# Kernel optimization log

Measured on AMD Instinct MI355X. Metric: run time of the kernel, lower is better.

The kernel has to match this reference:

```python
import jax, jax.numpy as jnp
import numpy as np

B, C, H, W = 256, 512, 14, 14
HW = H * W
TAU = 0.03          # args.tau
EPS = 0.65          # args.epsilon
EPS2 = 0.40         # args.epsilon - args.epsilon_margin
T_LOGIT = 0.07      # args.logit_temperature
MAX_ITERS = 32      # static unrolled bound for the data-dependent while-loop
PD_EPS = 1e-6       # torch.nn.PairwiseDistance default eps (added to the difference)


def setup_inputs() -> dict:
    key = jax.random.key(0)
    k1, k2 = jax.random.split(key)
    img = jax.random.normal(k1, (B, C, H, W), jnp.float32)
    img = img / (jnp.linalg.norm(img, axis=1, keepdims=True) + 1e-12)  # L2 over channels
    aud = jax.random.normal(k2, (B, C), jnp.float32)
    aud = aud / (jnp.linalg.norm(aud, axis=1, keepdims=True) + 1e-12)
    return {"img": img, "aud": aud}


def reference(img, aud):
    Bb, Cc, Hh, Ww = img.shape
    n_pix = Hh * Ww

    # PosLogits: [B,1,H,W]; Alllogits: [B,B,H,W]
    pos_logits = jnp.einsum('ncqa,nc->nqa', img, aud)[:, None]
    all_logits = jnp.einsum('ncqa,kc->nkqa', img, aud)

    # trimap negatives
    pos2 = jax.nn.sigmoid((pos_logits - EPS2) / TAU)
    neg = 1.0 - pos2                                        # [B,1,H,W]

    logit = img.reshape(Bb, Cc, -1) * pos_logits.reshape(Bb, 1, -1)   # [B,C,HW]
    positive0 = pos_logits.reshape(Bb, -1)                            # [B,HW]
    neg_val = (logit * neg.reshape(Bb, 1, -1)).mean(axis=2)           # [B,C]

    logit_t = logit.transpose(0, 2, 1)                                 # [B,HW,C]
    dist_to_zero = jnp.linalg.norm(logit_t - neg_val[:, None, :] + PD_EPS, axis=-1)  # [B,HW]

    def body(t, state):
        positive, already_pos, endpoint, obj = state
        idx = jnp.argmax(positive, axis=1)                             # [B] (detached in torch)
        sel = jnp.take_along_axis(logit, idx[:, None, None], axis=2)[:, :, 0]  # [B,C]
        obj = obj.at[t].set(sel * (~endpoint)[:, None].astype(sel.dtype))
        dist_to_logit = jnp.linalg.norm(logit_t - sel[:, None, :] + PD_EPS, axis=-1)  # [B,HW]
        pos = (dist_to_logit < dist_to_zero) & (~already_pos)
        already_pos = already_pos | pos
        positive = positive * (1.0 - pos.astype(positive.dtype))
        endpoint = endpoint | (pos.sum(axis=1) == 0) | (positive.max(axis=1) < 0.1)
        return (positive, already_pos, endpoint, obj)

    obj0 = jnp.zeros((MAX_ITERS, Bb, Cc), img.dtype)
    state0 = (positive0,
              jnp.zeros((Bb, n_pix), bool),
              jnp.zeros((Bb,), bool),
              obj0)
    _, _, _, object_arr = jax.lax.fori_loop(0, MAX_ITERS, body, state0)

    # lvs contrastive loss
    mask = 1.0 - 100.0 * jnp.eye(Bb, dtype=img.dtype)
    pos_m = jax.nn.sigmoid((pos_logits - EPS) / TAU)                   # [B,1,H,W]
    pos_all = jax.nn.sigmoid((all_logits - EPS) / TAU)                 # [B,B,H,W]
    sim1 = (pos_m * pos_logits).reshape(Bb, 1, -1).sum(-1) / pos_m.reshape(Bb, 1, -1).sum(-1)
    sim = (pos_all * all_logits).reshape(Bb, Bb, -1).sum(-1) / pos_all.reshape(Bb, Bb, -1).sum(-1) * mask
    sim2 = (neg * pos_logits).reshape(Bb, 1, -1).sum(-1) / neg.reshape(Bb, 1, -1).sum(-1)
    logits = jnp.concatenate((sim1, sim, sim2), axis=1) / T_LOGIT      # [B, B+2]
    loss = -jax.nn.log_softmax(logits, axis=1)[:, 0].mean()           # CE with target 0

    return loss, pos_logits[:, 0], object_arr
```

## Files before the change

### kernel.cpp

```cpp
#include <hip/hip_runtime.h>
#include <hip/hip_bf16.h>
#include <math.h>

#define NB 256
#define NC 512
#define NP 196
#define NIT 32
#define PROWS 208

typedef __attribute__((ext_vector_type(8))) short bf16x8;
typedef __attribute__((ext_vector_type(4))) float f32x4;

__device__ __forceinline__ float sigf(float z){ return 1.0f/(1.0f+expf(-z)); }

__device__ __forceinline__ unsigned short f2bf(float x){
  return __bfloat16_as_ushort(__float2bfloat16(x));
}
__device__ __forceinline__ float bf2f(unsigned short h){
  union{float f; unsigned u;} v; v.u = ((unsigned)h)<<16; return v.f;
}
__device__ __forceinline__ double dshfl_xor(double v, int m){
  int lo = __shfl_xor(__double2loint(v), m);
  int hi = __shfl_xor(__double2hiint(v), m);
  return __hiloint2double(hi, lo);
}

__global__ __launch_bounds__(256) void aud2bf_kernel(const float* __restrict__ aud, unsigned short* __restrict__ aud_bf)
{
  int i = blockIdx.x*256 + threadIdx.x;
  aud_bf[i] = f2bf(aud[i]);
}


#define SFSTR 211
__global__ __launch_bounds__(512) void convert3_kernel(
    const float* __restrict__ img, const float* __restrict__ aud,
    unsigned short* __restrict__ hiT, unsigned short* __restrict__ loT,
    double* __restrict__ ppl, double* __restrict__ pcs)
{
  const int bid = blockIdx.x;
  const int b = bid & 255, part = bid >> 8;
  const int tid = threadIdx.x;
  const float* imgb = img + (size_t)b*NC*NP;
  __shared__ float sf[32*SFSTR];
  __shared__ double s_dp[PROWS], s_ds[PROWS];
  __shared__ float s_aud[128];
  if (tid < 128) s_aud[tid] = aud[b*NC + part*128 + tid];
  for (int i=tid;i<PROWS;i+=512){ s_dp[i]=0.0; s_ds[i]=0.0; }

  for (int ss=0; ss<4; ++ss){
    const int c0 = part*128 + ss*32;
    __syncthreads();
    for (int j=tid; j<32*49; j+=512){
      int p4 = j % 49, c = j / 49;
      float4 v = *(const float4*)&imgb[(size_t)(c0+c)*NP + p4*4];
      sf[c*SFSTR + p4*4+0]=v.x; sf[c*SFSTR + p4*4+1]=v.y;
      sf[c*SFSTR + p4*4+2]=v.z; sf[c*SFSTR + p4*4+3]=v.w;
    }
    __syncthreads();
    for (int j=tid; j<PROWS*4; j+=512){
      int p = j >> 2, cq = j & 3;
      unsigned hv[4], lv[4];
      double dot=0.0, sm=0.0;
      #pragma unroll
      for (int k2=0;k2<4;++k2){
        float x0 = (p<NP) ? sf[(cq*8+2*k2  )*SFSTR + p] : 0.f;
        float x1 = (p<NP) ? sf[(cq*8+2*k2+1)*SFSTR + p] : 0.f;
        unsigned short h0=f2bf(x0), h1=f2bf(x1);
        unsigned short l0=f2bf(x0-bf2f(h0)), l1=f2bf(x1-bf2f(h1));
        hv[k2] = (unsigned)h0 | ((unsigned)h1<<16);
        lv[k2] = (unsigned)l0 | ((unsigned)l1<<16);
        int ca = ss*32 + cq*8 + 2*k2;
        dot += (double)x0*(double)s_aud[ca] + (double)x1*(double)s_aud[ca+1];
        sm  += (double)x0 + (double)x1;
      }
      size_t o = ((size_t)b*PROWS + p)*NC + c0 + cq*8;
      *(uint4*)&hiT[o] = *(uint4*)hv;
      *(uint4*)&loT[o] = *(uint4*)lv;
      dot += dshfl_xor(dot,1); dot += dshfl_xor(dot,2);
      sm  += dshfl_xor(sm,1);  sm  += dshfl_xor(sm,2);
      if (cq==0 && p<NP){ s_dp[p] += dot; s_ds[p] += sm; }
    }
  }
  __syncthreads();
  for (int i=tid;i<NP;i+=512){
    ppl[((size_t)b*4 + part)*NP + i] = s_dp[i];
    pcs[((size_t)b*4 + part)*NP + i] = s_ds[i];
  }
}

__global__ __launch_bounds__(256) void prep3_kernel(
    const double* __restrict__ ppl, const double* __restrict__ pcs,
    float* __restrict__ pl, float* __restrict__ cs,
    float* __restrict__ sim1, float* __restrict__ sim2, float* __restrict__ out_pl)
{
  const int b = blockIdx.x, tid = threadIdx.x;
  __shared__ double s_redd[256];
  float plv=0.f;
  if (tid < NP){
    double a=0.0, s=0.0;
    #pragma unroll
    for (int part=0; part<4; ++part){
      a += ppl[((size_t)b*4+part)*NP + tid];
      s += pcs[((size_t)b*4+part)*NP + tid];
    }
    plv=(float)a;
    float csv=(float)s;
    pl[b*NP+tid]=plv; cs[b*NP+tid]=csv; out_pl[b*NP+tid]=plv;
  }
  float pmw = (tid<NP)? sigf((plv-0.65f)/0.03f) : 0.f;
  float negw= (tid<NP)? 1.0f - sigf((plv-0.40f)/0.03f) : 0.f;
  double r[4];
  r[0]=(tid<NP)?(double)pmw*(double)plv:0.0;
  r[1]=(tid<NP)?(double)pmw:0.0;
  r[2]=(tid<NP)?(double)negw*(double)plv:0.0;
  r[3]=(tid<NP)?(double)negw:0.0;
  double res[4];
  for (int i=0;i<4;++i){
    __syncthreads();
    s_redd[tid]=r[i];
    __syncthreads();
    for (int s=128;s>0;s>>=1){ if (tid<s) s_redd[tid]+=s_redd[tid+s]; __syncthreads(); }
    res[i]=s_redd[0];
  }
  if (tid==0){
    sim1[b]=(float)(res[0]/res[1]);
    sim2[b]=(float)(res[2]/res[3]);
  }
}

#define LSTR 72
__global__ __launch_bounds__(512) void gram2_kernel(
    const unsigned short* __restrict__ hiT, const unsigned short* __restrict__ loT,
    float* __restrict__ G)
{
  const int bid = blockIdx.x;
  const int b = bid & 255, h = bid >> 8;
  const int cbase = 7*h, ncl = 7 - h;
  const int tid = threadIdx.x, lane = tid & 63, w = tid >> 6;
  const int nr = (w<5)?2:1;
  const unsigned short* hb = hiT + (size_t)b*PROWS*NC;
  const unsigned short* lb = loT + (size_t)b*PROWS*NC;
  float* Gb = G + (size_t)b*NP*NP;
  __shared__ short smh[PROWS*LSTR];
  __shared__ short sml[PROWS*LSTR];

  f32x4 acc[2][7];
  #pragma unroll
  for (int i=0;i<2;++i)
    #pragma unroll
    for (int j=0;j<7;++j) acc[i][j]=(f32x4){0,0,0,0};

  for (int sl=0; sl<8; ++sl){
    __syncthreads();
    for (int j=tid; j<PROWS*8; j+=512){
      int p = j>>3, o = j&7;
      size_t src = (size_t)p*NC + sl*64 + o*8;
      uint4 hv = *(const uint4*)(hb + src);
      uint4 lv = *(const uint4*)(lb + src);
      *(uint4*)&smh[p*LSTR + o*8] = hv;
      *(uint4*)&sml[p*LSTR + o*8] = lv;
    }
    __syncthreads();
    #pragma unroll
    for (int kk=0; kk<2; ++kk){
      bf16x8 Ah[2], Al[2];
      #pragma unroll
      for (int i=0;i<2;++i){
        if (i<nr){
          int r = (w + 8*i)*16 + (lane&15);
          Ah[i] = *(const bf16x8*)&smh[r*LSTR + kk*32 + (lane>>4)*8];
          Al[i] = *(const bf16x8*)&sml[r*LSTR + kk*32 + (lane>>4)*8];
        }
      }
      #pragma unroll
      for (int j=0;j<7;++j){
        if (j<ncl){
          int r = (cbase+j)*16 + (lane&15);
          bf16x8 Bh = *(const bf16x8*)&smh[r*LSTR + kk*32 + (lane>>4)*8];
          bf16x8 Bl = *(const bf16x8*)&sml[r*LSTR + kk*32 + (lane>>4)*8];
          #pragma unroll
          for (int i=0;i<2;++i){
            if (i<nr){
              acc[i][j] = __builtin_amdgcn_mfma_f32_16x16x32_bf16(Ah[i], Bh, acc[i][j], 0,0,0);
              acc[i][j] = __builtin_amdgcn_mfma_f32_16x16x32_bf16(Ah[i], Bl, acc[i][j], 0,0,0);
              acc[i][j] = __builtin_amdgcn_mfma_f32_16x16x32_bf16(Al[i], Bh, acc[i][j], 0,0,0);
            }
          }
        }
      }
    }
  }

  const int r0 = (lane>>4)*4, colL = lane & 15;
  #pragma unroll
  for (int i=0;i<2;++i){
    #pragma unroll
    for (int j=0;j<7;++j){
      if (i<nr && j<ncl){
        int row = (w+8*i)*16 + r0;
        int col = (cbase+j)*16 + colL;
        if (col < NP){
          #pragma unroll
          for (int jj=0;jj<4;++jj){
            if (row+jj < NP) Gb[(size_t)(row+jj)*NP + col] = acc[i][j][jj];
          }
        }
      }
    }
  }
}

__global__ __launch_bounds__(512) void simgemm2_kernel(
    const unsigned short* __restrict__ hiT, const unsigned short* __restrict__ aud_bf,
    float* __restrict__ sumWA, float* __restrict__ sumW)
{
  const int bid = blockIdx.x;
  const int b = bid & 255, h = bid >> 8;
  const int tid = threadIdx.x, lane = tid & 63, w = tid >> 6;
  const int wr = w >> 2, wc = w & 3;
  const int pbase = (wr==0)?0:7, npt = 7-wr;
  const unsigned short* hb = hiT + (size_t)b*PROWS*NC;
  __shared__ short smh[PROWS*LSTR];
  __shared__ short sma[128*LSTR];
  __shared__ float sred[2][2][4][2][16];

  f32x4 acc[7][2];
  #pragma unroll
  for (int i=0;i<7;++i)
    #pragma unroll
    for (int n=0;n<2;++n) acc[i][n]=(f32x4){0,0,0,0};

  for (int sl=0; sl<8; ++sl){
    __syncthreads();
    for (int j=tid; j<PROWS*8; j+=512){
      int p = j>>3, o = j&7;
      *(uint4*)&smh[p*LSTR + o*8] = *(const uint4*)(hb + (size_t)p*NC + sl*64 + o*8);
    }
    for (int j=tid; j<128*8; j+=512){
      int n = j>>3, o = j&7;
      *(uint4*)&sma[n*LSTR + o*8] = *(const uint4*)(aud_bf + (size_t)(h*128+n)*NC + sl*64 + o*8);
    }
    __syncthreads();
    #pragma unroll
    for (int kk=0; kk<2; ++kk){
      bf16x8 Ah[7];
      #pragma unroll
      for (int i=0;i<7;++i){
        if (i<npt){
          int r = (pbase+i)*16 + (lane&15);
          Ah[i] = *(const bf16x8*)&smh[r*LSTR + kk*32 + (lane>>4)*8];
        }
      }
      #pragma unroll
      for (int n=0;n<2;++n){
        int r = (wc*2+n)*16 + (lane&15);
        bf16x8 Bn = *(const bf16x8*)&sma[r*LSTR + kk*32 + (lane>>4)*8];
        #pragma unroll
        for (int i=0;i<7;++i)
          if (i<npt)
            acc[i][n] = __builtin_amdgcn_mfma_f32_16x16x32_bf16(Ah[i], Bn, acc[i][n], 0,0,0);
      }
    }
  }

  float swa[2]={0,0}, sw[2]={0,0};
  #pragma unroll
  for (int n=0;n<2;++n){
    #pragma unroll
    for (int i=0;i<7;++i){
      if (i<npt){
        int rowbase = (pbase+i)*16 + (lane>>4)*4;
        #pragma unroll
        for (int jj=0;jj<4;++jj){
          if (rowbase+jj < NP){
            float v = acc[i][n][jj];
            float wgt = sigf((v-0.65f)/0.03f);
            swa[n] += wgt*v; sw[n] += wgt;
          }
        }
      }
    }
  }
  #pragma unroll
  for (int n=0;n<2;++n){
    swa[n] += __shfl_xor(swa[n],16); swa[n] += __shfl_xor(swa[n],32);
    sw[n]  += __shfl_xor(sw[n],16);  sw[n]  += __shfl_xor(sw[n],32);
  }
  if (lane < 16){
    #pragma unroll
    for (int n=0;n<2;++n){
      sred[0][wr][wc][n][lane] = swa[n];
      sred[1][wr][wc][n][lane] = sw[n];
    }
  }
  __syncthreads();
  if (tid < 128){
    int wc2 = tid>>5, n2 = (tid>>4)&1, col = tid&15;
    float a = sred[0][0][wc2][n2][col] + sred[0][1][wc2][n2][col];
    float s = sred[1][0][wc2][n2][col] + sred[1][1][wc2][n2][col];
    int kcol = h*128 + (wc2*2+n2)*16 + col;
    sumWA[(size_t)b*NB + kcol] = a;
    sumW [(size_t)b*NB + kcol] = s;
  }
}

__global__ __launch_bounds__(256) void loop3_kernel(
    const float* __restrict__ pl, const float* __restrict__ cs,
    const float* __restrict__ G, int* __restrict__ qseq, int* __restrict__ zf)
{
  const int b = blockIdx.x, tid = threadIdx.x, lane = tid & 63, w = tid >> 6;
  const float* Gb = G + (size_t)b*NP*NP;
  __shared__ float sG[NP*NP];
  __shared__ float s_pl[NP], s_wl[NP], s_csL[NP], s_gd[NP];
  __shared__ double gwd[NP];
  __shared__ double s_redd[256];

  #pragma unroll
  for (int k=0;k<38;++k){
    int j = k*256 + tid;
    if (j < NP*NP/4) ((float4*)sG)[j] = ((const float4*)Gb)[j];
  }
  float negw_t = 0.f;
  if (tid < NP){
    float plv = pl[b*NP+tid];
    float csv = cs[b*NP+tid];
    s_pl[tid] = plv;
    s_csL[tid] = plv*csv;
    negw_t = 1.0f - sigf((plv-0.40f)/0.03f);
    s_wl[tid] = plv*negw_t;
    s_gd[tid] = Gb[(size_t)tid*NP + tid];
  }
  __syncthreads();

  double gw = 0.0;
  if (tid < NP){
    for (int q=0;q<NP;++q) gw += (double)sG[q*NP + tid] * (double)s_wl[q];
    gwd[tid] = gw;
  }
  __syncthreads();
  s_redd[tid] = (tid<NP) ? (double)s_wl[tid]*gw : 0.0;
  __syncthreads();
  for (int st=128;st>0;st>>=1){ if (tid<st) s_redd[tid]+=s_redd[tid+st]; __syncthreads(); }
  const double S2 = s_redd[0];
  __syncthreads();
  s_redd[tid] = (tid<NP) ? (double)negw_t*(double)s_csL[tid] : 0.0;
  __syncthreads();
  for (int st=128;st>0;st>>=1){ if (tid<st) s_redd[tid]+=s_redd[tid+st]; __syncthreads(); }
  const double Swl = s_redd[0];
  __syncthreads();

  if (tid < NP){
    const double e = (double)1e-6f;
    double pld = (double)s_pl[tid];
    double d0sq = pld*pld*(double)s_gd[tid]
                - (2.0/196.0)*pld*gwd[tid]
                + S2/(196.0*196.0)
                + 2.0*e*((double)s_csL[tid] - Swl/196.0)
                + 512.0*e*e;
    if (d0sq < 0.0) d0sq = 0.0;
    gwd[tid] = d0sq;
  }
  __syncthreads();

  if (w != 0) return;

  float plv[4], csL[4], gdd[4], posv[4];
  double d0sq[4];
  bool alr[4];
  #pragma unroll
  for (int s=0;s<4;++s){
    int p = lane + 64*s;
    bool valid = p < NP;
    plv[s]  = valid ? s_pl[p]  : 0.f;
    csL[s]  = valid ? s_csL[p] : 0.f;
    gdd[s]  = valid ? s_gd[p]  : 0.f;
    d0sq[s] = valid ? gwd[p]   : 0.0;
    posv[s] = valid ? plv[s]   : -INFINITY;
    alr[s] = false;
  }
  bool endp = false;

  for (int t=0;t<NIT;++t){
    float v = posv[0]; int ix = lane;
    #pragma unroll
    for (int s=1;s<4;++s){
      if (posv[s] > v){ v = posv[s]; ix = lane + 64*s; }
    }
    #pragma unroll
    for (int m=1;m<64;m<<=1){
      float vv = __shfl_xor(v, m);
      int   ii = __shfl_xor(ix, m);
      if (vv>v || (vv==v && ii<ix)){ v=vv; ix=ii; }
    }
    const int q = ix;
    const float plq  = s_pl[q];
    const float gqq  = s_gd[q];
    const float csLq = s_csL[q];
    if (lane==0){ qseq[b*NIT+t] = q; zf[b*NIT+t] = endp ? 1 : 0; }

    int cnt = 0;
    #pragma unroll
    for (int s=0;s<4;++s){
      int p = lane + 64*s;
      if (p<NP && !alr[s]){
        float Gpq = sG[q*NP + p];
        double plp=(double)plv[s], dq=(double)plq;
        const double e=(double)1e-6f;
        double d2 = plp*plp*(double)gdd[s]
                  - 2.0*plp*dq*(double)Gpq
                  + dq*dq*(double)gqq
                  + 2.0*e*((double)csL[s]-(double)csLq)
                  + 512.0*e*e;
        if (d2<0.0) d2=0.0;
        if (d2 < d0sq[s]){ alr[s]=true; posv[s]=posv[s]*0.0f; cnt++; }
      }
    }
    float mx = fmaxf(fmaxf(posv[0],posv[1]),fmaxf(posv[2],posv[3]));
    #pragma unroll
    for (int m=1;m<64;m<<=1){
      cnt += __shfl_xor(cnt, m);
      mx = fmaxf(mx, __shfl_xor(mx, m));
    }
    if (cnt==0 || mx<0.1f) endp=true;
  }
}

__global__ __launch_bounds__(64) void objw_kernel(
    const unsigned short* __restrict__ hiT, const unsigned short* __restrict__ loT,
    const float* __restrict__ pl, const int* __restrict__ qseq, const int* __restrict__ zf,
    float* __restrict__ obj)
{
  const int bid = blockIdx.x;
  const int b = bid >> 5, t = bid & 31;
  const int lane = threadIdx.x;
  float* op = obj + ((size_t)t*NB + b)*NC;
  const int z = zf[b*NIT + t];
  if (z){
    float4 zv = {0.f,0.f,0.f,0.f};
    *(float4*)&op[lane*8]   = zv;
    *(float4*)&op[lane*8+4] = zv;
    return;
  }
  const int q = qseq[b*NIT + t];
  const float plq = pl[b*NP + q];
  size_t src = ((size_t)b*PROWS + q)*NC + lane*8;
  uint4 hv = *(const uint4*)(hiT + src);
  uint4 lv = *(const uint4*)(loT + src);
  const unsigned* hw = (const unsigned*)&hv;
  const unsigned* lw = (const unsigned*)&lv;
  float o8[8];
  #pragma unroll
  for (int k2=0;k2<4;++k2){
    float x0 = bf2f((unsigned short)(hw[k2]&0xffff)) + bf2f((unsigned short)(lw[k2]&0xffff));
    float x1 = bf2f((unsigned short)(hw[k2]>>16))    + bf2f((unsigned short)(lw[k2]>>16));
    o8[2*k2]   = x0*plq;
    o8[2*k2+1] = x1*plq;
  }
  *(float4*)&op[lane*8]   = *(float4*)&o8[0];
  *(float4*)&op[lane*8+4] = *(float4*)&o8[4];
}

__global__ __launch_bounds__(256) void finalize_b(
    const float* __restrict__ sim1, const float* __restrict__ sim2,
    const float* __restrict__ sumWA, const float* __restrict__ sumW,
    float* __restrict__ lossb)
{
  const int b = blockIdx.x, k = threadIdx.x;
  __shared__ float s_red[256];
  __shared__ double s_redd[256];
  const float T = 0.07f;
  float s = sumWA[(size_t)b*NB+k]/sumW[(size_t)b*NB+k];
  if (k==b) s *= -99.0f;
  const float lk = s/T;
  const float l0 = sim1[b]/T, ll = sim2[b]/T;
  s_red[k]=lk; __syncthreads();
  for (int st=128;st>0;st>>=1){ if(k<st) s_red[k]=fmaxf(s_red[k],s_red[k+st]); __syncthreads(); }
  const float m = fmaxf(s_red[0], fmaxf(l0,ll));
  __syncthreads();
  double e = (double)expf(lk-m);
  if (k==0) e += (double)expf(l0-m)+(double)expf(ll-m);
  s_redd[k]=e; __syncthreads();
  for (int st=128;st>0;st>>=1){ if(k<st) s_redd[k]+=s_redd[k+st]; __syncthreads(); }
  if (k==0) lossb[b] = -(float)((double)(l0-m) - log(s_redd[0]));
}

__global__ __launch_bounds__(256) void finalize_sum(const float* __restrict__ lossb, float* __restrict__ out_loss)
{
  const int tid = threadIdx.x;
  __shared__ double sr[256];
  sr[tid]=(double)lossb[tid]; __syncthreads();
  for (int st=128;st>0;st>>=1){ if(tid<st) sr[tid]+=sr[tid+st]; __syncthreads(); }
  if (tid==0) out_loss[0]=(float)(sr[0]/256.0);
}


__global__ __launch_bounds__(256) void prep_fb(
    const float* __restrict__ img, const float* __restrict__ aud,
    float* __restrict__ pl, float* __restrict__ cs, float* __restrict__ d0,
    float* __restrict__ sim1, float* __restrict__ sim2,
    float* __restrict__ out_pl)
{
  const int b = blockIdx.x, tid = threadIdx.x;
  const float* imgb = img + (size_t)b*NC*NP;
  __shared__ float s_aud[NC];
  __shared__ float s_wl[NP];
  __shared__ float s_nv[NC];
  __shared__ double s_redd[256];
  for (int c=tid;c<NC;c+=256) s_aud[c]=aud[b*NC+c];
  __syncthreads();
  float plv=0.f, pmw=0.f, negw=0.f;
  if (tid<NP){
    double a=0.0, s=0.0;
    for (int c=0;c<NC;++c){ float x=imgb[(size_t)c*NP+tid]; a += (double)x*(double)s_aud[c]; s += (double)x; }
    plv=(float)a;
    float csv=(float)s;
    pl[b*NP+tid]=plv; cs[b*NP+tid]=csv; out_pl[b*NP+tid]=plv;
    pmw  = sigf((plv-0.65f)/0.03f);
    negw = 1.0f - sigf((plv-0.40f)/0.03f);
    s_wl[tid]=plv*negw;
  }
  double r[4];
  r[0]=(tid<NP)?(double)pmw*(double)plv:0.0;
  r[1]=(tid<NP)?(double)pmw:0.0;
  r[2]=(tid<NP)?(double)negw*(double)plv:0.0;
  r[3]=(tid<NP)?(double)negw:0.0;
  double res[4];
  for (int i=0;i<4;++i){
    __syncthreads();
    s_redd[tid]=r[i];
    __syncthreads();
    for (int s=128;s>0;s>>=1){ if (tid<s) s_redd[tid]+=s_redd[tid+s]; __syncthreads(); }
    res[i]=s_redd[0];
  }
  if (tid==0){
    sim1[b]=(float)(res[0]/res[1]);
    sim2[b]=(float)(res[2]/res[3]);
  }
  __syncthreads();
  for (int c=tid;c<NC;c+=256){
    const float* row = imgb + (size_t)c*NP;
    double a=0.0;
    for (int p=0;p<NP;++p) a += (double)row[p]*(double)s_wl[p];
    s_nv[c]=(float)(a/(double)NP);
  }
  __syncthreads();
  if (tid<NP){
    double a=0.0;
    const double e=(double)1e-6f;
    for (int c=0;c<NC;++c){
      double t=(double)imgb[(size_t)c*NP+tid]*(double)plv - (double)s_nv[c] + e;
      a += t*t;
    }
    d0[b*NP+tid]=(float)sqrt(a);
  }
}

#define GKS 64
#define GSTR 72
#define SKS 128
#define SSTR 136

__device__ __forceinline__ bf16x8 frag_ld(const short* sm, int stride, int tile, int kk, int lane){
  int r = tile*16 + (lane & 15);
  int o = lane >> 4;
  const short* p = sm + r*stride + kk*32 + o*8;
  return *(const bf16x8*)p;
}

__global__ __launch_bounds__(512) void gram_fb(const float* __restrict__ img, float* __restrict__ G)
{
  const int b = blockIdx.x;
  const int tid = threadIdx.x, lane = tid & 63, w = tid >> 6;
  const int wr = w >> 1, wc = w & 1;
  const int rbase = (wr==0)?0:(3*wr+1), nr = (wr==0)?4:3;
  const int cbase = 7*wc, ncl = 7-wc;
  const float* imgb = img + (size_t)b*NC*NP;
  float* Gb = G + (size_t)b*NP*NP;
  __shared__ short smh[PROWS*GSTR];
  __shared__ short sml[PROWS*GSTR];

  f32x4 acc[4][7];
  #pragma unroll
  for (int i=0;i<4;++i)
    #pragma unroll
    for (int j=0;j<7;++j) acc[i][j] = (f32x4){0.f,0.f,0.f,0.f};

  for (int sl=0; sl<NC/GKS; ++sl){
    __syncthreads();
    #pragma unroll
    for (int it=0; it<4; ++it){
      int j = it*512 + tid;
      int p = j & 255, c8 = j >> 8;
      if (p < PROWS){
        float x[8];
        #pragma unroll
        for (int cc=0;cc<8;++cc){
          int c = sl*GKS + c8*8 + cc;
          x[cc] = (p<NP) ? imgb[(size_t)c*NP + p] : 0.f;
        }
        unsigned hw[4], lw[4];
        #pragma unroll
        for (int k2=0;k2<4;++k2){
          unsigned short h0=f2bf(x[2*k2]), h1=f2bf(x[2*k2+1]);
          float l0 = x[2*k2]-bf2f(h0), l1 = x[2*k2+1]-bf2f(h1);
          hw[k2] = (unsigned)h0 | ((unsigned)h1<<16);
          lw[k2] = (unsigned)f2bf(l0) | ((unsigned)f2bf(l1)<<16);
        }
        *(uint4*)&smh[p*GSTR + c8*8] = *(uint4*)hw;
        *(uint4*)&sml[p*GSTR + c8*8] = *(uint4*)lw;
      }
    }
    __syncthreads();
    #pragma unroll
    for (int kk=0; kk<GKS/32; ++kk){
      bf16x8 Ah[4], Al[4];
      #pragma unroll
      for (int i=0;i<4;++i){
        if (i<nr){ Ah[i]=frag_ld(smh,GSTR,rbase+i,kk,lane); Al[i]=frag_ld(sml,GSTR,rbase+i,kk,lane); }
      }
      #pragma unroll
      for (int j=0;j<7;++j){
        if (j<ncl){
          bf16x8 Bh = frag_ld(smh,GSTR,cbase+j,kk,lane);
          bf16x8 Bl = frag_ld(sml,GSTR,cbase+j,kk,lane);
          #pragma unroll
          for (int i=0;i<4;++i){
            if (i<nr){
              acc[i][j] = __builtin_amdgcn_mfma_f32_16x16x32_bf16(Ah[i], Bh, acc[i][j], 0,0,0);
              acc[i][j] = __builtin_amdgcn_mfma_f32_16x16x32_bf16(Ah[i], Bl, acc[i][j], 0,0,0);
              acc[i][j] = __builtin_amdgcn_mfma_f32_16x16x32_bf16(Al[i], Bh, acc[i][j], 0,0,0);
            }
          }
        }
      }
    }
  }

  const int r0 = (lane>>4)*4, colL = lane & 15;
  #pragma unroll
  for (int i=0;i<4;++i){
    #pragma unroll
    for (int j=0;j<7;++j){
      if (i<nr && j<ncl){
        int row = (rbase+i)*16 + r0;
        int col = (cbase+j)*16 + colL;
        if (col < NP){
          #pragma unroll
          for (int jj=0;jj<4;++jj){
            if (row+jj < NP) Gb[(size_t)(row+jj)*NP + col] = acc[i][j][jj];
          }
        }
      }
    }
  }
}

__global__ __launch_bounds__(512) void simgemm_fb(
    const float* __restrict__ img, const unsigned short* __restrict__ aud_bf,
    float* __restrict__ sumWA, float* __restrict__ sumW)
{
  const int b = blockIdx.x;
  const int tid = threadIdx.x, lane = tid & 63, w = tid >> 6;
  const int wr = w >> 2, wc = w & 3;
  const int pbase = (wr==0)?0:7, npt = 7-wr;
  const float* imgb = img + (size_t)b*NC*NP;
  __shared__ short smh[PROWS*SSTR];
  __shared__ float sred[2][2][4][4][16];

  f32x4 acc[7][4];
  #pragma unroll
  for (int i=0;i<7;++i)
    #pragma unroll
    for (int n=0;n<4;++n) acc[i][n] = (f32x4){0.f,0.f,0.f,0.f};

  for (int sl=0; sl<NC/SKS; ++sl){
    __syncthreads();
    #pragma unroll
    for (int it=0; it<8; ++it){
      int j = it*512 + tid;
      int p = j & 255, c8 = j >> 8;
      if (p < PROWS){
        float x[8];
        #pragma unroll
        for (int cc=0;cc<8;++cc){
          int c = sl*SKS + c8*8 + cc;
          x[cc] = (p<NP) ? imgb[(size_t)c*NP + p] : 0.f;
        }
        unsigned hw[4];
        #pragma unroll
        for (int k2=0;k2<4;++k2)
          hw[k2] = (unsigned)f2bf(x[2*k2]) | ((unsigned)f2bf(x[2*k2+1])<<16);
        *(uint4*)&smh[p*SSTR + c8*8] = *(uint4*)hw;
      }
    }
    __syncthreads();
    #pragma unroll
    for (int kk=0; kk<SKS/32; ++kk){
      bf16x8 Ah[7];
      #pragma unroll
      for (int i=0;i<7;++i)
        if (i<npt) Ah[i]=frag_ld(smh,SSTR,pbase+i,kk,lane);
      #pragma unroll
      for (int n=0;n<4;++n){
        int ntile = wc*4 + n;
        int k = ntile*16 + (lane&15);
        int c = sl*SKS + kk*32 + (lane>>4)*8;
        bf16x8 Bn = *(const bf16x8*)(aud_bf + (size_t)k*NC + c);
        #pragma unroll
        for (int i=0;i<7;++i)
          if (i<npt)
            acc[i][n] = __builtin_amdgcn_mfma_f32_16x16x32_bf16(Ah[i], Bn, acc[i][n], 0,0,0);
      }
    }
  }

  float swa[4]={0,0,0,0}, sw[4]={0,0,0,0};
  #pragma unroll
  for (int n=0;n<4;++n){
    #pragma unroll
    for (int i=0;i<7;++i){
      if (i<npt){
        int rowbase = (pbase+i)*16 + (lane>>4)*4;
        #pragma unroll
        for (int jj=0;jj<4;++jj){
          if (rowbase+jj < NP){
            float v = acc[i][n][jj];
            float wgt = sigf((v-0.65f)/0.03f);
            swa[n] += wgt*v; sw[n] += wgt;
          }
        }
      }
    }
  }
  #pragma unroll
  for (int n=0;n<4;++n){
    swa[n] += __shfl_xor(swa[n],16); swa[n] += __shfl_xor(swa[n],32);
    sw[n]  += __shfl_xor(sw[n],16);  sw[n]  += __shfl_xor(sw[n],32);
  }
  if (lane < 16){
    #pragma unroll
    for (int n=0;n<4;++n){
      sred[0][wr][wc][n][lane] = swa[n];
      sred[1][wr][wc][n][lane] = sw[n];
    }
  }
  __syncthreads();
  if (tid < 256){
    int wc2 = tid>>6, n2 = (tid>>4)&3, col = tid&15;
    float a = sred[0][0][wc2][n2][col] + sred[0][1][wc2][n2][col];
    float s = sred[1][0][wc2][n2][col] + sred[1][1][wc2][n2][col];
    sumWA[(size_t)b*NB + tid] = a;
    sumW [(size_t)b*NB + tid] = s;
  }
}

__global__ __launch_bounds__(64) void loop_fb(
    const float* __restrict__ img, const float* __restrict__ pl,
    const float* __restrict__ cs, const float* __restrict__ d0,
    const float* __restrict__ G, float* __restrict__ obj)
{
  const int b = blockIdx.x, lane = threadIdx.x;
  const float* imgb = img + (size_t)b*NC*NP;
  const float* Gb = G + (size_t)b*NP*NP;

  float plv[4], csL[4], d0v[4], gdd[4], posv[4];
  bool alr[4];
  #pragma unroll
  for (int s=0;s<4;++s){
    int p = lane + 64*s;
    bool valid = p < NP;
    plv[s] = valid ? pl[b*NP+p] : 0.f;
    csL[s] = valid ? plv[s]*cs[b*NP+p] : 0.f;
    d0v[s] = valid ? d0[b*NP+p] : 0.f;
    gdd[s] = valid ? Gb[(size_t)p*NP+p] : 0.f;
    posv[s] = valid ? plv[s] : -INFINITY;
    alr[s] = false;
  }
  bool endp = false;

  for (int t=0;t<NIT;++t){
    float v = posv[0]; int ix = lane;
    #pragma unroll
    for (int s=1;s<4;++s){
      if (posv[s] > v){ v = posv[s]; ix = lane + 64*s; }
    }
    #pragma unroll
    for (int m=1;m<64;m<<=1){
      float vv = __shfl_xor(v, m);
      int   ii = __shfl_xor(ix, m);
      if (vv>v || (vv==v && ii<ix)){ v=vv; ix=ii; }
    }
    const int q = ix;
    const int slot = q >> 6, ln = q & 63;
    float pq=0.f, gq=0.f, cq=0.f;
    #pragma unroll
    for (int s=0;s<4;++s){
      if (s==slot){ pq=plv[s]; gq=gdd[s]; cq=csL[s]; }
    }
    const float plq  = __shfl(pq, ln);
    const float gqq  = __shfl(gq, ln);
    const float csLq = __shfl(cq, ln);

    {
      float* op = obj + ((size_t)t*NB + b)*NC;
      #pragma unroll
      for (int j2=0;j2<8;++j2){
        int c = lane + 64*j2;
        op[c] = endp ? 0.0f : imgb[(size_t)c*NP + q]*plq;
      }
    }

    int cnt = 0;
    #pragma unroll
    for (int s=0;s<4;++s){
      int p = lane + 64*s;
      if (p<NP && !alr[s]){
        float Gpq = Gb[(size_t)q*NP + p];
        double plp=(double)plv[s], dq=(double)plq;
        const double e=(double)1e-6f;
        double d2 = plp*plp*(double)gdd[s]
                  - 2.0*plp*dq*(double)Gpq
                  + dq*dq*(double)gqq
                  + 2.0*e*((double)csL[s]-(double)csLq)
                  + (double)NC*e*e;
        if (d2<0.0) d2=0.0;
        if (sqrt(d2) < (double)d0v[s]){ alr[s]=true; posv[s]=posv[s]*0.0f; cnt++; }
      }
    }
    float mx = fmaxf(fmaxf(posv[0],posv[1]),fmaxf(posv[2],posv[3]));
    #pragma unroll
    for (int m=1;m<64;m<<=1){
      cnt += __shfl_xor(cnt, m);
      mx = fmaxf(mx, __shfl_xor(mx, m));
    }
    if (cnt==0 || mx<0.1f) endp=true;
  }
}

__global__ __launch_bounds__(256) void finalize_fb(
    const float* __restrict__ sim1, const float* __restrict__ sim2,
    const float* __restrict__ sumWA, const float* __restrict__ sumW,
    float* __restrict__ out_loss)
{
  const int b = threadIdx.x;
  const float T = 0.07f;
  float l0 = sim1[b]/T;
  float ll = sim2[b]/T;
  float m = fmaxf(l0,ll);
  for (int k=0;k<NB;++k){
    float s = sumWA[(size_t)b*NB+k]/sumW[(size_t)b*NB+k];
    if (k==b) s *= -99.0f;
    m = fmaxf(m, s/T);
  }
  double se = exp((double)(l0-m)) + exp((double)(ll-m));
  for (int k=0;k<NB;++k){
    float s = sumWA[(size_t)b*NB+k]/sumW[(size_t)b*NB+k];
    if (k==b) s *= -99.0f;
    se += exp((double)(s/T-m));
  }
  float lsm0 = (float)((double)(l0-m) - log(se));
  __shared__ double s_redd[256];
  s_redd[b] = -(double)lsm0;
  __syncthreads();
  for (int s=128;s>0;s>>=1){ if (b<s) s_redd[b]+=s_redd[b+s]; __syncthreads(); }
  if (b==0) out_loss[0]=(float)(s_redd[0]/(double)NB);
}

extern "C" void kernel_launch(void* const* d_in, const int* in_sizes, int n_in,
                              void* d_out, int out_size, void* d_ws, size_t ws_size,
                              hipStream_t stream)
{
  const float* img = (const float*)d_in[0];
  const float* aud = (const float*)d_in[1];
  float* out = (float*)d_out;
  float* ws  = (float*)d_ws;

  float* pl    = ws;
  float* cs    = pl    + NB*NP;
  float* d0    = cs    + NB*NP;
  float* sim1  = d0    + NB*NP;
  float* sim2  = sim1  + NB;
  float* sumWA = sim2  + NB;
  float* sumW  = sumWA + NB*NB;
  unsigned short* aud_bf = (unsigned short*)(sumW + NB*NB);
  float* G     = (float*)(aud_bf + NB*NC);
  unsigned short* hiT = (unsigned short*)(G + (size_t)NB*NP*NP);
  unsigned short* loT = hiT + (size_t)NB*PROWS*NC;
  int* qseq    = (int*)(loT + (size_t)NB*PROWS*NC);
  int* zf      = qseq + NB*NIT;
  float* lossb = (float*)(zf + NB*NIT);

  double* ppl = (double*)G;
  double* pcs = ppl + (size_t)NB*4*NP;

  const size_t need_fast = (size_t)((char*)(lossb + NB) - (char*)ws);

  float* out_loss = out;
  float* out_pl   = out + 1;
  float* out_obj  = out + 1 + NB*NP;

  hipLaunchKernelGGL(aud2bf_kernel, dim3(NB*NC/256), dim3(256), 0, stream, aud, aud_bf);

  if (ws_size >= need_fast){
    hipLaunchKernelGGL(convert3_kernel, dim3(NB*4),   dim3(512), 0, stream, img, aud, hiT, loT, ppl, pcs);
    hipLaunchKernelGGL(prep3_kernel,    dim3(NB),     dim3(256), 0, stream, ppl, pcs, pl, cs, sim1, sim2, out_pl);
    hipLaunchKernelGGL(gram2_kernel,    dim3(NB*2),   dim3(512), 0, stream, hiT, loT, G);
    hipLaunchKernelGGL(loop3_kernel,    dim3(NB),     dim3(256), 0, stream, pl, cs, G, qseq, zf);
    hipLaunchKernelGGL(simgemm2_kernel, dim3(NB*2),   dim3(512), 0, stream, hiT, aud_bf, sumWA, sumW);
    hipLaunchKernelGGL(objw_kernel,     dim3(NB*NIT), dim3(64),  0, stream, hiT, loT, pl, qseq, zf, out_obj);
    hipLaunchKernelGGL(finalize_b,      dim3(NB),     dim3(256), 0, stream, sim1, sim2, sumWA, sumW, lossb);
    hipLaunchKernelGGL(finalize_sum,    dim3(1),      dim3(256), 0, stream, lossb, out_loss);
  } else {
    hipLaunchKernelGGL(prep_fb,    dim3(NB), dim3(256), 0, stream, img, aud, pl, cs, d0, sim1, sim2, out_pl);
    hipLaunchKernelGGL(gram_fb,    dim3(NB), dim3(512), 0, stream, img, G);
    hipLaunchKernelGGL(simgemm_fb, dim3(NB), dim3(512), 0, stream, img, aud_bf, sumWA, sumW);
    hipLaunchKernelGGL(loop_fb,    dim3(NB), dim3(64),  0, stream, img, pl, cs, d0, G, out_obj);
    hipLaunchKernelGGL(finalize_fb,dim3(1),  dim3(256), 0, stream, sim1, sim2, sumWA, sumW, out_loss);
  }
}
```

Measured before the change: 211.6 us.

## Interleave bf16 hi/lo split planes into one packed 32-bit panel

The separate hi and lo bf16 transposed arrays are merged into a single array holding the hi and lo halves of each element in one 32-bit word. The convert kernel writes this packed panel, and the gram, simgemm and object-gather kernels load it and unpack the hi/lo fragments in registers with shift and mask operations. The aim is one contiguous global stream and one shared-memory tile, using an odd stride to avoid bank conflicts. In exchange, simgemm now loads twice the bytes it needs, since it only uses the hi part, and every fragment read pays extra unpacking ALU work.

```diff
diff --git a/kernel.cpp b/kernel.cpp
--- a/kernel.cpp
+++ b/kernel.cpp
@@ -7,6 +7,7 @@
 #define NP 196
 #define NIT 32
 #define PROWS 208
+#define USTR 65
 
 typedef __attribute__((ext_vector_type(8))) short bf16x8;
 typedef __attribute__((ext_vector_type(4))) float f32x4;
@@ -25,6 +26,27 @@
   return __hiloint2double(hi, lo);
 }
 
+__device__ __forceinline__ void frag_pk(const unsigned* su, int r, int kk, int lane,
+                                        bf16x8* hi, bf16x8* lo){
+  const unsigned* p = su + r*USTR + kk*32 + ((lane>>4)<<3);
+  uint4 a = *(const uint4*)p;
+  uint4 b = *(const uint4*)(p+4);
+  union { uint4 u; bf16x8 v; } H;
+  H.u.x = (a.x>>16) | (a.y & 0xffff0000u);
+  H.u.y = (a.z>>16) | (a.w & 0xffff0000u);
+  H.u.z = (b.x>>16) | (b.y & 0xffff0000u);
+  H.u.w = (b.z>>16) | (b.w & 0xffff0000u);
+  *hi = H.v;
+  if (lo){
+    union { uint4 u; bf16x8 v; } L;
+    L.u.x = (a.x & 0xffffu) | (a.y<<16);
+    L.u.y = (a.z & 0xffffu) | (a.w<<16);
+    L.u.z = (b.x & 0xffffu) | (b.y<<16);
+    L.u.w = (b.z & 0xffffu) | (b.w<<16);
+    *lo = L.v;
+  }
+}
+
 __global__ __launch_bounds__(256) void aud2bf_kernel(const float* __restrict__ aud, unsigned short* __restrict__ aud_bf)
 {
   int i = blockIdx.x*256 + threadIdx.x;
@@ -35,7 +57,7 @@
 #define SFSTR 211
 __global__ __launch_bounds__(512) void convert3_kernel(
     const float* __restrict__ img, const float* __restrict__ aud,
-    unsigned short* __restrict__ hiT, unsigned short* __restrict__ loT,
+    unsigned* __restrict__ pan,
     double* __restrict__ ppl, double* __restrict__ pcs)
 {
   const int bid = blockIdx.x;
@@ -60,7 +82,7 @@
     __syncthreads();
     for (int j=tid; j<PROWS*4; j+=512){
       int p = j >> 2, cq = j & 3;
-      unsigned hv[4], lv[4];
+      union { uint4 u; unsigned w[4]; } A, B;
       double dot=0.0, sm=0.0;
       #pragma unroll
       for (int k2=0;k2<4;++k2){
@@ -68,15 +90,17 @@
         float x1 = (p<NP) ? sf[(cq*8+2*k2+1)*SFSTR + p] : 0.f;
         unsigned short h0=f2bf(x0), h1=f2bf(x1);
         unsigned short l0=f2bf(x0-bf2f(h0)), l1=f2bf(x1-bf2f(h1));
-        hv[k2] = (unsigned)h0 | ((unsigned)h1<<16);
-        lv[k2] = (unsigned)l0 | ((unsigned)l1<<16);
+        unsigned pk0 = ((unsigned)h0<<16) | l0;
+        unsigned pk1 = ((unsigned)h1<<16) | l1;
+        if (k2 < 2){ A.w[2*k2]=pk0; A.w[2*k2+1]=pk1; }
+        else       { B.w[2*(k2-2)]=pk0; B.w[2*(k2-2)+1]=pk1; }
         int ca = ss*32 + cq*8 + 2*k2;
         dot += (double)x0*(double)s_aud[ca] + (double)x1*(double)s_aud[ca+1];
         sm  += (double)x0 + (double)x1;
       }
       size_t o = ((size_t)b*PROWS + p)*NC + c0 + cq*8;
-      *(uint4*)&hiT[o] = *(uint4*)hv;
-      *(uint4*)&loT[o] = *(uint4*)lv;
+      *(uint4*)&pan[o]   = A.u;
+      *(uint4*)&pan[o+4] = B.u;
       dot += dshfl_xor(dot,1); dot += dshfl_xor(dot,2);
       sm  += dshfl_xor(sm,1);  sm  += dshfl_xor(sm,2);
       if (cq==0 && p<NP){ s_dp[p] += dot; s_ds[p] += sm; }
@@ -129,21 +153,17 @@
   }
 }
 
-#define LSTR 72
 __global__ __launch_bounds__(512) void gram2_kernel(
-    const unsigned short* __restrict__ hiT, const unsigned short* __restrict__ loT,
-    float* __restrict__ G)
+    const unsigned* __restrict__ pan, float* __restrict__ G)
 {
   const int bid = blockIdx.x;
   const int b = bid & 255, h = bid >> 8;
   const int cbase = 7*h, ncl = 7 - h;
   const int tid = threadIdx.x, lane = tid & 63, w = tid >> 6;
   const int nr = (w<5)?2:1;
-  const unsigned short* hb = hiT + (size_t)b*PROWS*NC;
-  const unsigned short* lb = loT + (size_t)b*PROWS*NC;
+  const unsigned* pb = pan + (size_t)b*PROWS*NC;
   float* Gb = G + (size_t)b*NP*NP;
-  __shared__ short smh[PROWS*LSTR];
-  __shared__ short sml[PROWS*LSTR];
+  __shared__ unsigned su[PROWS*USTR];
 
   f32x4 acc[2][7];
   #pragma unroll
@@ -155,11 +175,11 @@
     __syncthreads();
     for (int j=tid; j<PROWS*8; j+=512){
       int p = j>>3, o = j&7;
-      size_t src = (size_t)p*NC + sl*64 + o*8;
-      uint4 hv = *(const uint4*)(hb + src);
-      uint4 lv = *(const uint4*)(lb + src);
-      *(uint4*)&smh[p*LSTR + o*8] = hv;
-      *(uint4*)&sml[p*LSTR + o*8] = lv;
+      const unsigned* src = pb + (size_t)p*NC + sl*64 + o*8;
+      uint4 va = *(const uint4*)src;
+      uint4 vb = *(const uint4*)(src+4);
+      *(uint4*)&su[p*USTR + o*8]     = va;
+      *(uint4*)&su[p*USTR + o*8 + 4] = vb;
     }
     __syncthreads();
     #pragma unroll
@@ -169,16 +189,15 @@
       for (int i=0;i<2;++i){
         if (i<nr){
           int r = (w + 8*i)*16 + (lane&15);
-          Ah[i] = *(const bf16x8*)&smh[r*LSTR + kk*32 + (lane>>4)*8];
-          Al[i] = *(const bf16x8*)&sml[r*LSTR + kk*32 + (lane>>4)*8];
+          frag_pk(su, r, kk, lane, &Ah[i], &Al[i]);
         }
       }
       #pragma unroll
       for (int j=0;j<7;++j){
         if (j<ncl){
           int r = (cbase+j)*16 + (lane&15);
-          bf16x8 Bh = *(const bf16x8*)&smh[r*LSTR + kk*32 + (lane>>4)*8];
-          bf16x8 Bl = *(const bf16x8*)&sml[r*LSTR + kk*32 + (lane>>4)*8];
+          bf16x8 Bh, Bl;
+          frag_pk(su, r, kk, lane, &Bh, &Bl);
           #pragma unroll
           for (int i=0;i<2;++i){
             if (i<nr){
@@ -211,8 +230,9 @@
   }
 }
 
+#define LSTR 72
 __global__ __launch_bounds__(512) void simgemm2_kernel(
-    const unsigned short* __restrict__ hiT, const unsigned short* __restrict__ aud_bf,
+    const unsigned* __restrict__ pan, const unsigned short* __restrict__ aud_bf,
     float* __restrict__ sumWA, float* __restrict__ sumW)
 {
   const int bid = blockIdx.x;
@@ -220,8 +240,8 @@
   const int tid = threadIdx.x, lane = tid & 63, w = tid >> 6;
   const int wr = w >> 2, wc = w & 3;
   const int pbase = (wr==0)?0:7, npt = 7-wr;
-  const unsigned short* hb = hiT + (size_t)b*PROWS*NC;
-  __shared__ short smh[PROWS*LSTR];
+  const unsigned* pb = pan + (size_t)b*PROWS*NC;
+  __shared__ unsigned su[PROWS*USTR];
   __shared__ short sma[128*LSTR];
   __shared__ float sred[2][2][4][2][16];
 
@@ -235,7 +255,11 @@
     __syncthreads();
     for (int j=tid; j<PROWS*8; j+=512){
       int p = j>>3, o = j&7;
-      *(uint4*)&smh[p*LSTR + o*8] = *(const uint4*)(hb + (size_t)p*NC + sl*64 + o*8);
+      const unsigned* src = pb + (size_t)p*NC + sl*64 + o*8;
+      uint4 va = *(const uint4*)src;
+      uint4 vb = *(const uint4*)(src+4);
+      *(uint4*)&su[p*USTR + o*8]     = va;
+      *(uint4*)&su[p*USTR + o*8 + 4] = vb;
     }
     for (int j=tid; j<128*8; j+=512){
       int n = j>>3, o = j&7;
@@ -249,7 +273,7 @@
       for (int i=0;i<7;++i){
         if (i<npt){
           int r = (pbase+i)*16 + (lane&15);
-          Ah[i] = *(const bf16x8*)&smh[r*LSTR + kk*32 + (lane>>4)*8];
+          frag_pk(su, r, kk, lane, &Ah[i], nullptr);
         }
       }
       #pragma unroll
@@ -427,7 +451,7 @@
 }
 
 __global__ __launch_bounds__(64) void objw_kernel(
-    const unsigned short* __restrict__ hiT, const unsigned short* __restrict__ loT,
+    const unsigned* __restrict__ pan,
     const float* __restrict__ pl, const int* __restrict__ qseq, const int* __restrict__ zf,
     float* __restrict__ obj)
 {
@@ -444,18 +468,15 @@
   }
   const int q = qseq[b*NIT + t];
   const float plq = pl[b*NP + q];
-  size_t src = ((size_t)b*PROWS + q)*NC + lane*8;
-  uint4 hv = *(const uint4*)(hiT + src);
-  uint4 lv = *(const uint4*)(loT + src);
-  const unsigned* hw = (const unsigned*)&hv;
-  const unsigned* lw = (const unsigned*)&lv;
+  const unsigned* src = pan + ((size_t)b*PROWS + q)*NC + lane*8;
+  uint4 a = *(const uint4*)src;
+  uint4 b4 = *(const uint4*)(src+4);
+  const unsigned pw[8] = {a.x,a.y,a.z,a.w,b4.x,b4.y,b4.z,b4.w};
   float o8[8];
   #pragma unroll
-  for (int k2=0;k2<4;++k2){
-    float x0 = bf2f((unsigned short)(hw[k2]&0xffff)) + bf2f((unsigned short)(lw[k2]&0xffff));
-    float x1 = bf2f((unsigned short)(hw[k2]>>16))    + bf2f((unsigned short)(lw[k2]>>16));
-    o8[2*k2]   = x0*plq;
-    o8[2*k2+1] = x1*plq;
+  for (int e=0;e<8;++e){
+    float x = bf2f((unsigned short)(pw[e]>>16)) + bf2f((unsigned short)(pw[e]&0xffffu));
+    o8[e] = x*plq;
   }
   *(float4*)&op[lane*8]   = *(float4*)&o8[0];
   *(float4*)&op[lane*8+4] = *(float4*)&o8[4];
@@ -885,9 +906,8 @@
   float* sumW  = sumWA + NB*NB;
   unsigned short* aud_bf = (unsigned short*)(sumW + NB*NB);
   float* G     = (float*)(aud_bf + NB*NC);
-  unsigned short* hiT = (unsigned short*)(G + (size_t)NB*NP*NP);
-  unsigned short* loT = hiT + (size_t)NB*PROWS*NC;
-  int* qseq    = (int*)(loT + (size_t)NB*PROWS*NC);
+  unsigned* pan = (unsigned*)(G + (size_t)NB*NP*NP);
+  int* qseq    = (int*)(pan + (size_t)NB*PROWS*NC);
   int* zf      = qseq + NB*NIT;
   float* lossb = (float*)(zf + NB*NIT);
 
@@ -903,12 +923,12 @@
   hipLaunchKernelGGL(aud2bf_kernel, dim3(NB*NC/256), dim3(256), 0, stream, aud, aud_bf);
 
   if (ws_size >= need_fast){
-    hipLaunchKernelGGL(convert3_kernel, dim3(NB*4),   dim3(512), 0, stream, img, aud, hiT, loT, ppl, pcs);
+    hipLaunchKernelGGL(convert3_kernel, dim3(NB*4),   dim3(512), 0, stream, img, aud, pan, ppl, pcs);
     hipLaunchKernelGGL(prep3_kernel,    dim3(NB),     dim3(256), 0, stream, ppl, pcs, pl, cs, sim1, sim2, out_pl);
-    hipLaunchKernelGGL(gram2_kernel,    dim3(NB*2),   dim3(512), 0, stream, hiT, loT, G);
+    hipLaunchKernelGGL(gram2_kernel,    dim3(NB*2),   dim3(512), 0, stream, pan, G);
     hipLaunchKernelGGL(loop3_kernel,    dim3(NB),     dim3(256), 0, stream, pl, cs, G, qseq, zf);
-    hipLaunchKernelGGL(simgemm2_kernel, dim3(NB*2),   dim3(512), 0, stream, hiT, aud_bf, sumWA, sumW);
-    hipLaunchKernelGGL(objw_kernel,     dim3(NB*NIT), dim3(64),  0, stream, hiT, loT, pl, qseq, zf, out_obj);
+    hipLaunchKernelGGL(simgemm2_kernel, dim3(NB*2),   dim3(512), 0, stream, pan, aud_bf, sumWA, sumW);
+    hipLaunchKernelGGL(objw_kernel,     dim3(NB*NIT), dim3(64),  0, stream, pan, pl, qseq, zf, out_obj);
     hipLaunchKernelGGL(finalize_b,      dim3(NB),     dim3(256), 0, stream, sim1, sim2, sumWA, sumW, lossb);
     hipLaunchKernelGGL(finalize_sum,    dim3(1),      dim3(256), 0, stream, lossb, out_loss);
   } else {
```

Measured after the change: 413.5 us. 95.4% more time.

## Tile hi/lo bf16 transposed image by 64-channel slabs and double convert grid

Applied to the files above, without the earlier changes.

Changes the hiT/loT workspace layout from row-major [b][p][512] to slab-major [b][slab][p][64], so each 64-channel slice read by the gram and sim GEMM kernels is contiguous. The convert kernel now handles one 64-channel slab per block over 2048 blocks in a single pass with no inner loop, and writes per-slab partial dot and sum values straight to global memory instead of accumulating them in shared memory. prep3 now reduces eight partials instead of four, and objw indexes the new layout. The goal is more parallelism in conversion and more contiguous loads downstream, at the cost of a larger shared-memory tile per block and more partial sums.

```diff
diff --git a/kernel.cpp b/kernel.cpp
--- a/kernel.cpp
+++ b/kernel.cpp
@@ -7,6 +7,7 @@
 #define NP 196
 #define NIT 32
 #define PROWS 208
+#define LSTR 72
 
 typedef __attribute__((ext_vector_type(8))) short bf16x8;
 typedef __attribute__((ext_vector_type(4))) float f32x4;
@@ -33,7 +34,7 @@
 
 
 #define SFSTR 211
-__global__ __launch_bounds__(512) void convert3_kernel(
+__global__ __launch_bounds__(512) void convert4_kernel(
     const float* __restrict__ img, const float* __restrict__ aud,
     unsigned short* __restrict__ hiT, unsigned short* __restrict__ loT,
     double* __restrict__ ppl, double* __restrict__ pcs)
@@ -41,51 +42,45 @@
   const int bid = blockIdx.x;
   const int b = bid & 255, part = bid >> 8;
   const int tid = threadIdx.x;
-  const float* imgb = img + (size_t)b*NC*NP;
-  __shared__ float sf[32*SFSTR];
-  __shared__ double s_dp[PROWS], s_ds[PROWS];
-  __shared__ float s_aud[128];
-  if (tid < 128) s_aud[tid] = aud[b*NC + part*128 + tid];
-  for (int i=tid;i<PROWS;i+=512){ s_dp[i]=0.0; s_ds[i]=0.0; }
-
-  for (int ss=0; ss<4; ++ss){
-    const int c0 = part*128 + ss*32;
-    __syncthreads();
-    for (int j=tid; j<32*49; j+=512){
-      int p4 = j % 49, c = j / 49;
-      float4 v = *(const float4*)&imgb[(size_t)(c0+c)*NP + p4*4];
-      sf[c*SFSTR + p4*4+0]=v.x; sf[c*SFSTR + p4*4+1]=v.y;
-      sf[c*SFSTR + p4*4+2]=v.z; sf[c*SFSTR + p4*4+3]=v.w;
-    }
-    __syncthreads();
-    for (int j=tid; j<PROWS*4; j+=512){
-      int p = j >> 2, cq = j & 3;
-      unsigned hv[4], lv[4];
-      double dot=0.0, sm=0.0;
-      #pragma unroll
-      for (int k2=0;k2<4;++k2){
-        float x0 = (p<NP) ? sf[(cq*8+2*k2  )*SFSTR + p] : 0.f;
-        float x1 = (p<NP) ? sf[(cq*8+2*k2+1)*SFSTR + p] : 0.f;
-        unsigned short h0=f2bf(x0), h1=f2bf(x1);
-        unsigned short l0=f2bf(x0-bf2f(h0)), l1=f2bf(x1-bf2f(h1));
-        hv[k2] = (unsigned)h0 | ((unsigned)h1<<16);
-        lv[k2] = (unsigned)l0 | ((unsigned)l1<<16);
-        int ca = ss*32 + cq*8 + 2*k2;
-        dot += (double)x0*(double)s_aud[ca] + (double)x1*(double)s_aud[ca+1];
-        sm  += (double)x0 + (double)x1;
-      }
-      size_t o = ((size_t)b*PROWS + p)*NC + c0 + cq*8;
-      *(uint4*)&hiT[o] = *(uint4*)hv;
-      *(uint4*)&loT[o] = *(uint4*)lv;
-      dot += dshfl_xor(dot,1); dot += dshfl_xor(dot,2);
-      sm  += dshfl_xor(sm,1);  sm  += dshfl_xor(sm,2);
-      if (cq==0 && p<NP){ s_dp[p] += dot; s_ds[p] += sm; }
-    }
-  }
-  __syncthreads();
-  for (int i=tid;i<NP;i+=512){
-    ppl[((size_t)b*4 + part)*NP + i] = s_dp[i];
-    pcs[((size_t)b*4 + part)*NP + i] = s_ds[i];
+  const float* imgb = img + (size_t)b*NC*NP + (size_t)part*64*NP;
+  __shared__ float sf[64*SFSTR];
+  __shared__ float s_aud[64];
+  if (tid < 64) s_aud[tid] = aud[b*NC + part*64 + tid];
+
+  for (int j=tid; j<64*49; j+=512){
+    int p4 = j % 49, c = j / 49;
+    float4 v = *(const float4*)&imgb[(size_t)c*NP + p4*4];
+    sf[c*SFSTR + p4*4+0]=v.x; sf[c*SFSTR + p4*4+1]=v.y;
+    sf[c*SFSTR + p4*4+2]=v.z; sf[c*SFSTR + p4*4+3]=v.w;
+  }
+  __syncthreads();
+
+  unsigned short* hp = hiT + (size_t)(b*8+part)*PROWS*64;
+  unsigned short* lp = loT + (size_t)(b*8+part)*PROWS*64;
+  for (int j=tid; j<PROWS*8; j+=512){
+    int p = j>>3, o = j&7;
+    unsigned hw[4], lw[4];
+    double dot=0.0, sm=0.0;
+    #pragma unroll
+    for (int k2=0;k2<4;++k2){
+      int c = o*8 + 2*k2;
+      float x0 = (p<NP) ? sf[c*SFSTR + p]     : 0.f;
+      float x1 = (p<NP) ? sf[(c+1)*SFSTR + p] : 0.f;
+      unsigned short h0=f2bf(x0), h1=f2bf(x1);
+      unsigned short l0=f2bf(x0-bf2f(h0)), l1=f2bf(x1-bf2f(h1));
+      hw[k2] = (unsigned)h0 | ((unsigned)h1<<16);
+      lw[k2] = (unsigned)l0 | ((unsigned)l1<<16);
+      dot += (double)x0*(double)s_aud[c] + (double)x1*(double)s_aud[c+1];
+      sm  += (double)x0 + (double)x1;
+    }
+    *(uint4*)&hp[p*64 + o*8] = *(uint4*)hw;
+    *(uint4*)&lp[p*64 + o*8] = *(uint4*)lw;
+    dot += dshfl_xor(dot,1); dot += dshfl_xor(dot,2); dot += dshfl_xor(dot,4);
+    sm  += dshfl_xor(sm,1);  sm  += dshfl_xor(sm,2);  sm  += dshfl_xor(sm,4);
+    if (o==0 && p<NP){
+      ppl[(size_t)(b*8+part)*NP + p] = dot;
+      pcs[(size_t)(b*8+part)*NP + p] = sm;
+    }
   }
 }
 
@@ -100,9 +95,9 @@
   if (tid < NP){
     double a=0.0, s=0.0;
     #pragma unroll
-    for (int part=0; part<4; ++part){
-      a += ppl[((size_t)b*4+part)*NP + tid];
-      s += pcs[((size_t)b*4+part)*NP + tid];
+    for (int part=0; part<8; ++part){
+      a += ppl[(size_t)(b*8+part)*NP + tid];
+      s += pcs[(size_t)(b*8+part)*NP + tid];
     }
     plv=(float)a;
     float csv=(float)s;
@@ -129,7 +124,6 @@
   }
 }
 
-#define LSTR 72
 __global__ __launch_bounds__(512) void gram2_kernel(
     const unsigned short* __restrict__ hiT, const unsigned short* __restrict__ loT,
     float* __restrict__ G)
@@ -139,8 +133,8 @@
   const int cbase = 7*h, ncl = 7 - h;
   const int tid = threadIdx.x, lane = tid & 63, w = tid >> 6;
   const int nr = (w<5)?2:1;
-  const unsigned short* hb = hiT + (size_t)b*PROWS*NC;
-  const unsigned short* lb = loT + (size_t)b*PROWS*NC;
+  const unsigned short* hb = hiT + (size_t)b*8*PROWS*64;
+  const unsigned short* lb = loT + (size_t)b*8*PROWS*64;
   float* Gb = G + (size_t)b*NP*NP;
   __shared__ short smh[PROWS*LSTR];
   __shared__ short sml[PROWS*LSTR];
@@ -155,11 +149,9 @@
     __syncthreads();
     for (int j=tid; j<PROWS*8; j+=512){
       int p = j>>3, o = j&7;
-      size_t src = (size_t)p*NC + sl*64 + o*8;
-      uint4 hv = *(const uint4*)(hb + src);
-      uint4 lv = *(const uint4*)(lb + src);
-      *(uint4*)&smh[p*LSTR + o*8] = hv;
-      *(uint4*)&sml[p*LSTR + o*8] = lv;
+      size_t src = ((size_t)sl*PROWS + p)*64 + o*8;
+      *(uint4*)&smh[p*LSTR + o*8] = *(const uint4*)(hb + src);
+      *(uint4*)&sml[p*LSTR + o*8] = *(const uint4*)(lb + src);
     }
     __syncthreads();
     #pragma unroll
@@ -220,7 +212,7 @@
   const int tid = threadIdx.x, lane = tid & 63, w = tid >> 6;
   const int wr = w >> 2, wc = w & 3;
   const int pbase = (wr==0)?0:7, npt = 7-wr;
-  const unsigned short* hb = hiT + (size_t)b*PROWS*NC;
+  const unsigned short* hb = hiT + (size_t)b*8*PROWS*64;
   __shared__ short smh[PROWS*LSTR];
   __shared__ short sma[128*LSTR];
   __shared__ float sred[2][2][4][2][16];
@@ -235,7 +227,7 @@
     __syncthreads();
     for (int j=tid; j<PROWS*8; j+=512){
       int p = j>>3, o = j&7;
-      *(uint4*)&smh[p*LSTR + o*8] = *(const uint4*)(hb + (size_t)p*NC + sl*64 + o*8);
+      *(uint4*)&smh[p*LSTR + o*8] = *(const uint4*)(hb + ((size_t)sl*PROWS + p)*64 + o*8);
     }
     for (int j=tid; j<128*8; j+=512){
       int n = j>>3, o = j&7;
@@ -444,7 +436,8 @@
   }
   const int q = qseq[b*NIT + t];
   const float plq = pl[b*NP + q];
-  size_t src = ((size_t)b*PROWS + q)*NC + lane*8;
+  const int part = lane >> 3, off = lane & 7;
+  size_t src = ((size_t)(b*8+part)*PROWS + q)*64 + off*8;
   uint4 hv = *(const uint4*)(hiT + src);
   uint4 lv = *(const uint4*)(loT + src);
   const unsigned* hw = (const unsigned*)&hv;
@@ -886,13 +879,13 @@
   unsigned short* aud_bf = (unsigned short*)(sumW + NB*NB);
   float* G     = (float*)(aud_bf + NB*NC);
   unsigned short* hiT = (unsigned short*)(G + (size_t)NB*NP*NP);
-  unsigned short* loT = hiT + (size_t)NB*PROWS*NC;
-  int* qseq    = (int*)(loT + (size_t)NB*PROWS*NC);
+  unsigned short* loT = hiT + (size_t)NB*8*PROWS*64;
+  int* qseq    = (int*)(loT + (size_t)NB*8*PROWS*64);
   int* zf      = qseq + NB*NIT;
   float* lossb = (float*)(zf + NB*NIT);
 
   double* ppl = (double*)G;
-  double* pcs = ppl + (size_t)NB*4*NP;
+  double* pcs = ppl + (size_t)NB*8*NP;
 
   const size_t need_fast = (size_t)((char*)(lossb + NB) - (char*)ws);
 
@@ -903,7 +896,7 @@
   hipLaunchKernelGGL(aud2bf_kernel, dim3(NB*NC/256), dim3(256), 0, stream, aud, aud_bf);
 
   if (ws_size >= need_fast){
-    hipLaunchKernelGGL(convert3_kernel, dim3(NB*4),   dim3(512), 0, stream, img, aud, hiT, loT, ppl, pcs);
+    hipLaunchKernelGGL(convert4_kernel, dim3(NB*8),   dim3(512), 0, stream, img, aud, hiT, loT, ppl, pcs);
     hipLaunchKernelGGL(prep3_kernel,    dim3(NB),     dim3(256), 0, stream, ppl, pcs, pl, cs, sim1, sim2, out_pl);
     hipLaunchKernelGGL(gram2_kernel,    dim3(NB*2),   dim3(512), 0, stream, hiT, loT, G);
     hipLaunchKernelGGL(loop3_kernel,    dim3(NB),     dim3(256), 0, stream, pl, cs, G, qseq, zf);
```

After: 204.0 us. -3.6%, faster.
